# Kernel optimization log

Hardware: AMD Instinct MI355X
Metric: run time of the kernel (lower is better)

## Reference

```python
import math
import jax, jax.numpy as jnp
import numpy as np

B, S, D, H = 2, 2048, 1024, 16
HD = D // H


def setup_inputs() -> dict:
    key = jax.random.key(0)
    ks = jax.random.split(key, 12)
    w = lambda k: jax.random.normal(k, (D, D), jnp.float32) * 0.02
    return {
        "query": jax.random.normal(ks[0], (B, S, D), jnp.float32),
        "key": jax.random.normal(ks[1], (B, S, D), jnp.float32),
        "value": jax.random.normal(ks[2], (B, S, D), jnp.float32),
        "mask": jax.random.randint(ks[3], (B, 1, S, S), 0, 2, jnp.int32),
        "relative_pos_bias": jax.random.normal(ks[4], (S, S, H), jnp.float32) * 0.1,
        "Wq": w(ks[5]), "bq": jnp.zeros((D,), jnp.float32),
        "Wk": w(ks[6]), "bk": jnp.zeros((D,), jnp.float32),
        "Wv": w(ks[7]), "bv": jnp.zeros((D,), jnp.float32),
        "Wo": w(ks[8]), "bo": jnp.zeros((D,), jnp.float32),
    }


def reference(query, key, value, mask, relative_pos_bias,
              Wq, bq, Wk, bk, Wv, bv, Wo, bo):
    b, s, d = query.shape
    h = relative_pos_bias.shape[-1]
    hd = d // h
    scale = math.sqrt(hd)
    # projections -> (b, h, s, hd)
    split = lambda x: x.reshape(b, s, h, hd).transpose(0, 2, 1, 3)
    Q = split(query @ Wq + bq)
    K = split(key @ Wk + bk)
    V = split(value @ Wv + bv)
    scores = jnp.einsum("bhqd,bhkd->bhqk", Q, K) / scale
    # torch: bias.unsqueeze(0).transpose(1,3) => scores[b,h,i,j] += bias[j,i,h]
    scores = scores + jnp.transpose(relative_pos_bias, (2, 1, 0))[None]
    scores = jnp.where(mask == 0, jnp.float32(-1e9), scores)
    attn = jax.nn.softmax(scores, axis=-1)
    out = jnp.einsum("bhqk,bhkd->bhqd", attn, V)
    out = out.transpose(0, 2, 1, 3).reshape(b, s, d)
    return out @ Wo + bo
```

## Files before the change

kernel.cpp:

```cpp
#include <hip/hip_runtime.h>
#include <math.h>

#define SS 2048
#define DD 1024
#define HH 16

typedef _Float16 f16;
typedef _Float16 half8 __attribute__((ext_vector_type(8)));
typedef _Float16 half4 __attribute__((ext_vector_type(4)));
typedef float f32x4 __attribute__((ext_vector_type(4)));
typedef unsigned long long u64;

#define LOG2E 1.44269504f
#define MASKNEG -30000.0f

__device__ __forceinline__ void gload16(const void* g, void* lds) {
    __builtin_amdgcn_global_load_lds(
        (const __attribute__((address_space(1))) unsigned int*)g,
        (__attribute__((address_space(3))) unsigned int*)lds, 16, 0, 0);
}

__global__ __launch_bounds__(256)
void prep_xw(const float* __restrict__ q, const float* __restrict__ k,
             const float* __restrict__ v, f16* __restrict__ oq,
             f16* __restrict__ ok, f16* __restrict__ ov,
             const float* __restrict__ wq, const float* __restrict__ wk,
             const float* __restrict__ wv, const float* __restrict__ wo,
             f16* __restrict__ owq, f16* __restrict__ owk,
             f16* __restrict__ owv, f16* __restrict__ owo)
{
    __shared__ __align__(16) char smem[16640];
    const int bid = blockIdx.x;
    const int t = threadIdx.x;
    if (bid < 6144) {
        const int z = bid / 2048, bx = bid % 2048;
        const float* src = z == 0 ? q : z == 1 ? k : v;
        f16* dst = z == 0 ? oq : z == 1 ? ok : ov;
        size_t i = ((size_t)bx * 256 + t) * 8;
        float4 v0 = *reinterpret_cast<const float4*>(src + i);
        float4 v1 = *reinterpret_cast<const float4*>(src + i + 4);
        half8 h;
        h[0] = (f16)v0.x; h[1] = (f16)v0.y; h[2] = (f16)v0.z; h[3] = (f16)v0.w;
        h[4] = (f16)v1.x; h[5] = (f16)v1.y; h[6] = (f16)v1.z; h[7] = (f16)v1.w;
        *reinterpret_cast<half8*>(dst + i) = h;
    } else {
        const int r = bid - 6144;
        const int z = r / 256;
        const int bx = r % 16, by = (r / 16) % 16;
        const float* W = z == 0 ? wq : z == 1 ? wk : z == 2 ? wv : wo;
        f16* WT = z == 0 ? owq : z == 1 ? owk : z == 2 ? owv : owo;
        float (*Lt)[65] = (float (*)[65])smem;
        const int n0 = bx * 64, k0 = by * 64;
        {
            int row = t >> 2;
            int c0  = (t & 3) * 16;
#pragma unroll
            for (int u = 0; u < 4; ++u) {
                float4 x = *reinterpret_cast<const float4*>(
                    &W[(size_t)(k0 + row) * DD + n0 + c0 + u * 4]);
                Lt[row][c0 + u * 4 + 0] = x.x;
                Lt[row][c0 + u * 4 + 1] = x.y;
                Lt[row][c0 + u * 4 + 2] = x.z;
                Lt[row][c0 + u * 4 + 3] = x.w;
            }
        }
        __syncthreads();
        {
            int n  = t >> 2;
            int kc = (t & 3) * 16;
            half8 h0, h1;
#pragma unroll
            for (int u = 0; u < 8; ++u) h0[u] = (f16)Lt[kc + u][n];
#pragma unroll
            for (int u = 0; u < 8; ++u) h1[u] = (f16)Lt[kc + 8 + u][n];
            f16* dst = &WT[(size_t)(n0 + n) * DD + k0 + kc];
            *reinterpret_cast<half8*>(dst) = h0;
            *reinterpret_cast<half8*>(dst + 8) = h1;
        }
    }
}

__device__ void proj3_body(char* smem, int gx, int gy, int gz,
                           const f16* Xq, const f16* Xk, const f16* Xv,
                           const f16* WqT, const f16* WkT, const f16* WvT,
                           const float* bq, const float* bk, const float* bv,
                           f16* Qo, f16* Ko, f16* VTo)
{
    char* AsB = smem;
    char* BsB = smem + 128 * 64 * 2;
    const int t = threadIdx.x, wid = t >> 6, l = t & 63, c = l & 15, g = l >> 4;
    const f16 *Ap, *Bp; const float* bias; int m0, n0;
    if (gz == 2) { Ap = WvT; Bp = Xv; bias = bv; m0 = gx * 128; n0 = gy * 128; }
    else if (gz == 1) { Ap = Xk; Bp = WkT; bias = bk; m0 = gy * 128; n0 = gx * 128; }
    else { Ap = Xq; Bp = WqT; bias = bq; m0 = gy * 128; n0 = gx * 128; }
    const int wm = wid >> 1, wn = wid & 1;
    f32x4 acc[4][4] = {};

    const int s  = l & 7;
    const int r0 = wid * 32 + (l >> 3);
    const int sdst = (s << 4) ^ ((r0 & 7) << 4);

    half8 aN[4], bN[4];
#pragma unroll
    for (int j = 0; j < 4; ++j) {
        int row = r0 + j * 8;
        aN[j] = *(const half8*)(Ap + (size_t)(m0 + row) * DD + s * 8);
        bN[j] = *(const half8*)(Bp + (size_t)(n0 + row) * DD + s * 8);
    }
#pragma unroll
    for (int j = 0; j < 4; ++j) {
        int row = r0 + j * 8;
        *(half8*)(AsB + row * 128 + sdst) = aN[j];
        *(half8*)(BsB + row * 128 + sdst) = bN[j];
    }
    __syncthreads();

    for (int k0 = 0; k0 < DD; k0 += 64) {
        const bool more = (k0 + 64 < DD);
        const int kn = more ? k0 + 64 : 0;
#pragma unroll
        for (int j = 0; j < 4; ++j) {
            int row = r0 + j * 8;
            aN[j] = *(const half8*)(Ap + (size_t)(m0 + row) * DD + kn + s * 8);
            bN[j] = *(const half8*)(Bp + (size_t)(n0 + row) * DD + kn + s * 8);
        }
#pragma unroll
        for (int ks = 0; ks < 2; ++ks) {
            half8 af[4];
#pragma unroll
            for (int mt = 0; mt < 4; ++mt) {
                int row = wm * 64 + mt * 16 + c;
                af[mt] = *(const half8*)(AsB + row * 128 +
                         ((ks * 64 + g * 16) ^ ((row & 7) << 4)));
            }
#pragma unroll
            for (int nt = 0; nt < 4; ++nt) {
                int row = wn * 64 + nt * 16 + c;
                half8 bf = *(const half8*)(BsB + row * 128 +
                           ((ks * 64 + g * 16) ^ ((row & 7) << 4)));
#pragma unroll
                for (int mt = 0; mt < 4; ++mt)
                    acc[mt][nt] = __builtin_amdgcn_mfma_f32_16x16x32_f16(
                        af[mt], bf, acc[mt][nt], 0, 0, 0);
            }
        }
        __syncthreads();
        if (more) {
#pragma unroll
            for (int j = 0; j < 4; ++j) {
                int row = r0 + j * 8;
                *(half8*)(AsB + row * 128 + sdst) = aN[j];
                *(half8*)(BsB + row * 128 + sdst) = bN[j];
            }
        }
        __syncthreads();
    }

    f16* Ls = (f16*)smem;
    const float post = (gz == 0) ? 0.125f * LOG2E : 1.0f;
    if (gz < 2) {
#pragma unroll
        for (int nt = 0; nt < 4; ++nt) {
            int col = wn * 64 + nt * 16 + c;
            float bn = bias[n0 + col];
#pragma unroll
            for (int mt = 0; mt < 4; ++mt)
#pragma unroll
                for (int reg = 0; reg < 4; ++reg) {
                    int row = wm * 64 + mt * 16 + 4 * g + reg;
                    Ls[row * 128 + (col ^ ((row & 7) << 3))] =
                        (f16)((acc[mt][nt][reg] + bn) * post);
                }
        }
    } else {
#pragma unroll
        for (int mt = 0; mt < 4; ++mt)
#pragma unroll
            for (int reg = 0; reg < 4; ++reg) {
                int row = wm * 64 + mt * 16 + 4 * g + reg;
                float bd = bias[m0 + row];
#pragma unroll
                for (int nt = 0; nt < 4; ++nt) {
                    int col = wn * 64 + nt * 16 + c;
                    Ls[row * 128 + (col ^ ((row & 7) << 3))] =
                        (f16)(acc[mt][nt][reg] + bd);
                }
            }
    }
    __syncthreads();
#pragma unroll
    for (int e = 0; e < 8; ++e) {
        int fi = e * 256 + t;
        int row = fi >> 4;
        int col0 = (fi & 15) * 8;
        half8 v = *reinterpret_cast<const half8*>(
            Ls + row * 128 + (col0 ^ ((row & 7) << 3)));
        if (gz < 2) {
            f16* dst = gz ? Ko : Qo;
            int m = m0 + row, n = n0 + col0;
            int b = m >> 11, sdx = m & (SS - 1);
            int h = n >> 6, hd = n & 63;
            *reinterpret_cast<half8*>(
                &dst[(((size_t)(b * HH + h)) * SS + sdx) * 64 + hd]) = v;
        } else {
            int m = m0 + row, n = n0 + col0;
            int h = m >> 6, dl = m & 63;
            int b = n >> 11;
            *reinterpret_cast<half8*>(
                &VTo[(((size_t)(b * HH + h)) * 64 + dl) * SS + (n & (SS - 1))]) = v;
        }
    }
}

__device__ void rpbT3_body(char* smem, int gxi, int gyj,
                           const float* rpb, f16* rpbT)
{
    f16* Lt = (f16*)smem;
    const int t = threadIdx.x, wid = t >> 6, l = t & 63;
    const int i0 = gxi * 16;
    const int j0 = gyj * 64;
    const int il = l >> 2;
    const int h0 = (l & 3) * 4;
    const int swz = (il & 7) << 3;
#pragma unroll
    for (int p = 0; p < 16; ++p) {
        int jl = p * 4 + wid;
        float4 v = *reinterpret_cast<const float4*>(
            rpb + ((size_t)(j0 + jl) * SS + i0 + il) * HH + h0);
        int js = jl ^ swz;
        Lt[((h0 + 0) * 16 + il) * 64 + js] = (f16)(v.x * LOG2E);
        Lt[((h0 + 1) * 16 + il) * 64 + js] = (f16)(v.y * LOG2E);
        Lt[((h0 + 2) * 16 + il) * 64 + js] = (f16)(v.z * LOG2E);
        Lt[((h0 + 3) * 16 + il) * 64 + js] = (f16)(v.w * LOG2E);
    }
    __syncthreads();
    const int part = t & 7;
#pragma unroll
    for (int p = 0; p < 8; ++p) {
        int rowid = p * 32 + (t >> 3);
        int h = rowid >> 4, i2 = rowid & 15;
        int rsw = (i2 & 7) << 3;
        const f16* rowp = Lt + (h * 16 + i2) * 64;
        half8 v;
#pragma unroll
        for (int e = 0; e < 8; ++e) {
            int sig = 32 * (part & 1) + 16 * (e >> 2) + 4 * (part >> 1) + (e & 3);
            v[e] = rowp[sig ^ rsw];
        }
        *reinterpret_cast<half8*>(
            rpbT + ((size_t)h * SS + i0 + i2) * SS + j0 + part * 8) = v;
    }
}

__device__ void maskbits_body(int gx, const int* mask, u64* mb)
{
    const int t = threadIdx.x, wid = t >> 6, l = t & 63;
    const int row = gx * 4 + wid;
    const int* src = mask + (size_t)row * SS;
    u64* dst = mb + (size_t)row * 32;
    for (int it = 0; it < 32; ++it) {
        int mv = src[it * 64 + l];
        u64 bal = __ballot(mv != 0);
        if (l == 0) dst[it] = bal;
    }
}

__global__ __launch_bounds__(256)
void prep_big(const f16* __restrict__ Xq, const f16* __restrict__ Xk,
              const f16* __restrict__ Xv, const f16* __restrict__ WqT,
              const f16* __restrict__ WkT, const f16* __restrict__ WvT,
              const float* __restrict__ bq, const float* __restrict__ bk,
              const float* __restrict__ bv,
              f16* __restrict__ Qo, f16* __restrict__ Ko, f16* __restrict__ VTo,
              const float* __restrict__ rpb, f16* __restrict__ rpbT,
              const int* __restrict__ mask, u64* __restrict__ mbits)
{
    __shared__ __align__(16) char smem[32768];
    const int bid = blockIdx.x;
    const int pid0 = (int)(((long long)bid * 768) / 5888);
    const int pid1 = (int)(((long long)(bid + 1) * 768) / 5888);
    if (pid1 != pid0) {
        proj3_body(smem, pid0 % 8, (pid0 / 8) % 32, pid0 / 256,
                   Xq, Xk, Xv, WqT, WkT, WvT, bq, bk, bv, Qo, Ko, VTo);
    } else {
        const int mid = bid - pid0;
        if (mid < 4096)
            rpbT3_body(smem, mid % 128, mid / 128, rpb, rpbT);
        else
            maskbits_body(mid - 4096, mask, mbits);
    }
}

__global__ __launch_bounds__(256, 4)
void attn_fwd(const f16* __restrict__ Qw, const f16* __restrict__ Kw,
              const f16* __restrict__ VTw, const f16* __restrict__ rpbT,
              const u64* __restrict__ mbits, f16* __restrict__ AOh)
{
    __shared__ f16 Ks[2][64 * 64];
    __shared__ f16 Vs[2][64 * 64];

    const int t = threadIdx.x, wid = t >> 6, l = t & 63, c = l & 15, g = l >> 4;
    const int bh = blockIdx.x, b = bh >> 4, h = bh & 15;
    const int q0 = blockIdx.y * 64;
    const size_t baseSD = (size_t)bh * SS * 64;
    const size_t baseDS = (size_t)bh * 64 * SS;
    const f16* Kbase = Kw + baseSD;
    const f16* Vbase = VTw + baseDS;

    const int qrow_c = q0 + wid * 16 + c;
    const f16* bp = rpbT + (size_t)h * SS * SS + (size_t)qrow_c * SS + g * 16;
    const u64* mp = mbits + ((size_t)b * SS + qrow_c) * 32;

    const int s     = l & 7;
    const int srow0 = wid * 16 + (l >> 3);
    const int sswz  = (srow0 & 7) << 4;
    const int kdst  = (s << 4) ^ sswz;
    const int velo  = 32 * (s >> 2) + 16 * (s & 1) + 4 * ((s >> 1) & 1);
    const int vdlo  = (velo * 2) ^ sswz;
    const int vdhi  = (velo * 2 + 16) ^ sswz;

    int ga[4];
#pragma unroll
    for (int r = 0; r < 4; ++r) ga[r] = (g * 4 + r) * 4;

    half8 qf[2];
    qf[0] = *(const half8*)(Qw + baseSD + (size_t)qrow_c * 64 + g * 8);
    qf[1] = *(const half8*)(Qw + baseSD + (size_t)qrow_c * 64 + 32 + g * 8);

    {
        half8 k0 = *(const half8*)(Kbase + (size_t)srow0 * 64 + s * 8);
        half8 k1 = *(const half8*)(Kbase + (size_t)(srow0 + 8) * 64 + s * 8);
        half8 v0 = *(const half8*)(Vbase + (size_t)srow0 * SS + s * 8);
        half8 v1 = *(const half8*)(Vbase + (size_t)(srow0 + 8) * SS + s * 8);
        char* kd = (char*)Ks[0]; char* vd = (char*)Vs[0];
        *(half8*)(kd + srow0 * 128 + kdst) = k0;
        *(half8*)(kd + (srow0 + 8) * 128 + kdst) = k1;
        half4 lo0 = {v0[0], v0[1], v0[2], v0[3]}, hi0 = {v0[4], v0[5], v0[6], v0[7]};
        half4 lo1 = {v1[0], v1[1], v1[2], v1[3]}, hi1 = {v1[4], v1[5], v1[6], v1[7]};
        *(half4*)(vd + srow0 * 128 + vdlo) = lo0;
        *(half4*)(vd + srow0 * 128 + vdhi) = hi0;
        *(half4*)(vd + (srow0 + 8) * 128 + vdlo) = lo1;
        *(half4*)(vd + (srow0 + 8) * 128 + vdhi) = hi1;
    }
    half8 bb0 = *(const half8*)(bp);
    half8 bb1 = *(const half8*)(bp + 8);
    u64 mm = mp[0];
    __syncthreads();

    f32x4 acc[4] = {};
    float mrow = -INFINITY, lp = 0.f;
    const int shg = 4 * g;

    int buf = 0;
    for (int kt = 0; kt < SS / 64; ++kt) {
        const bool more = (kt + 1 < SS / 64);
        const int jn = more ? (kt + 1) * 64 : 0;
        const int ktn = more ? kt + 1 : 0;

        half8 k0n = *(const half8*)(Kbase + (size_t)(jn + srow0) * 64 + s * 8);
        half8 k1n = *(const half8*)(Kbase + (size_t)(jn + srow0 + 8) * 64 + s * 8);
        half8 v0n = *(const half8*)(Vbase + (size_t)srow0 * SS + jn + s * 8);
        half8 v1n = *(const half8*)(Vbase + (size_t)(srow0 + 8) * SS + jn + s * 8);
        half8 bbn0 = *(const half8*)(bp + jn);
        half8 bbn1 = *(const half8*)(bp + jn + 8);
        u64 mmn = mp[ktn];

        char* KsB = (char*)Ks[buf];
        char* VsB = (char*)Vs[buf];

        u64 sh = mm >> shg;
        f32x4 sc[4];
#pragma unroll
        for (int nt = 0; nt < 4; ++nt)
#pragma unroll
            for (int r = 0; r < 4; ++r) {
                float bf = (float)(nt < 2 ? bb0[nt * 4 + r] : bb1[(nt - 2) * 4 + r]);
                sc[nt][r] = ((sh >> (16 * nt + r)) & 1) ? bf : MASKNEG;
            }

        __builtin_amdgcn_s_setprio(1);
#pragma unroll
        for (int ks = 0; ks < 2; ++ks)
#pragma unroll
            for (int nt = 0; nt < 4; ++nt) {
                int row = nt * 16 + c;
                half8 kf = *(const half8*)(KsB + row * 128 +
                           ((ks * 64 + g * 16) ^ ((row & 7) << 4)));
                sc[nt] = __builtin_amdgcn_mfma_f32_16x16x32_f16(
                    kf, qf[ks], sc[nt], 0, 0, 0);
            }
        __builtin_amdgcn_s_setprio(0);

        float rm = fmaxf(fmaxf(fmaxf(sc[0][0], sc[0][1]), fmaxf(sc[0][2], sc[0][3])),
                         fmaxf(fmaxf(sc[1][0], sc[1][1]), fmaxf(sc[1][2], sc[1][3])));
        rm = fmaxf(rm, fmaxf(fmaxf(fmaxf(sc[2][0], sc[2][1]), fmaxf(sc[2][2], sc[2][3])),
                             fmaxf(fmaxf(sc[3][0], sc[3][1]), fmaxf(sc[3][2], sc[3][3]))));
        rm = fmaxf(rm, __shfl_xor(rm, 16));
        rm = fmaxf(rm, __shfl_xor(rm, 32));
        if (!__all(rm <= mrow + 8.0f)) {
            float mn = fmaxf(mrow, rm);
            float scal = exp2f(mrow - mn);
            mrow = mn;
            lp *= scal;
            float sq[4];
#pragma unroll
            for (int r = 0; r < 4; ++r)
                sq[r] = __int_as_float(__builtin_amdgcn_ds_bpermute(
                            ga[r], __float_as_int(scal)));
#pragma unroll
            for (int nt = 0; nt < 4; ++nt)
#pragma unroll
                for (int r = 0; r < 4; ++r) acc[nt][r] *= sq[r];
        }
        float psum = 0.f;
#pragma unroll
        for (int nt = 0; nt < 4; ++nt)
#pragma unroll
            for (int r = 0; r < 4; ++r) {
                float p = exp2f(sc[nt][r] - mrow);
                sc[nt][r] = p;
                psum += p;
            }
        lp += psum;

        half4 pa[4];
#pragma unroll
        for (int kk = 0; kk < 4; ++kk) {
            half4 pv = {(f16)sc[kk][0], (f16)sc[kk][1],
                        (f16)sc[kk][2], (f16)sc[kk][3]};
            pa[kk] = pv;
        }

        __builtin_amdgcn_s_setprio(1);
#pragma unroll
        for (int ks = 0; ks < 2; ++ks)
#pragma unroll
            for (int nt2 = 0; nt2 < 4; ++nt2) {
                int row = nt2 * 16 + c;
                half8 vf = *(const half8*)(VsB + row * 128 +
                           ((ks * 64 + g * 16) ^ ((row & 7) << 4)));
                half4 vlo = {vf[0], vf[1], vf[2], vf[3]};
                half4 vhi = {vf[4], vf[5], vf[6], vf[7]};
                acc[nt2] = __builtin_amdgcn_mfma_f32_16x16x16f16(
                    pa[2 * ks], vlo, acc[nt2], 0, 0, 0);
                acc[nt2] = __builtin_amdgcn_mfma_f32_16x16x16f16(
                    pa[2 * ks + 1], vhi, acc[nt2], 0, 0, 0);
            }
        __builtin_amdgcn_s_setprio(0);

        if (more) {
            char* kd = (char*)Ks[buf ^ 1];
            char* vd = (char*)Vs[buf ^ 1];
            *(half8*)(kd + srow0 * 128 + kdst) = k0n;
            *(half8*)(kd + (srow0 + 8) * 128 + kdst) = k1n;
            half4 lo0 = {v0n[0], v0n[1], v0n[2], v0n[3]}, hi0 = {v0n[4], v0n[5], v0n[6], v0n[7]};
            half4 lo1 = {v1n[0], v1n[1], v1n[2], v1n[3]}, hi1 = {v1n[4], v1n[5], v1n[6], v1n[7]};
            *(half4*)(vd + srow0 * 128 + vdlo) = lo0;
            *(half4*)(vd + srow0 * 128 + vdhi) = hi0;
            *(half4*)(vd + (srow0 + 8) * 128 + vdlo) = lo1;
            *(half4*)(vd + (srow0 + 8) * 128 + vdhi) = hi1;
            buf ^= 1;
            bb0 = bbn0; bb1 = bbn1; mm = mmn;
        }
        __syncthreads();
    }

    float lt = lp;
    lt += __shfl_xor(lt, 16);
    lt += __shfl_xor(lt, 32);
    float linv[4];
#pragma unroll
    for (int r = 0; r < 4; ++r)
        linv[r] = 1.0f / __int_as_float(__builtin_amdgcn_ds_bpermute(
                      ga[r], __float_as_int(lt)));
#pragma unroll
    for (int r = 0; r < 4; ++r) {
        int qrow = q0 + wid * 16 + 4 * g + r;
#pragma unroll
        for (int nt2 = 0; nt2 < 4; ++nt2)
            AOh[((size_t)b * SS + qrow) * DD + h * 64 + nt2 * 16 + c] =
                (f16)(acc[nt2][r] * linv[r]);
    }
}

__global__ __launch_bounds__(256)
void gemm_out(const f16* __restrict__ A, const f16* __restrict__ BT,
              const float* __restrict__ bias, float* __restrict__ out)
{
    __shared__ f16 As[128 * 64];
    __shared__ f16 Bs[128 * 64];
    const int t = threadIdx.x, wid = t >> 6, l = t & 63, c = l & 15, g = l >> 4;
    const int m0 = blockIdx.y * 128, n0 = blockIdx.x * 128;
    const int wm = wid >> 1, wn = wid & 1;
    f32x4 acc[4][4] = {};
    char* AsB = (char*)As; char* BsB = (char*)Bs;

    for (int k0 = 0; k0 < DD; k0 += 64) {
        __syncthreads();
#pragma unroll
        for (int j = 0; j < 4; ++j) {
            int row = wid * 32 + j * 8 + (l >> 3);
            int slot = (l & 7) ^ (row & 7);
            gload16(A + (size_t)(m0 + row) * DD + k0 + slot * 8,
                    AsB + (wid * 32 + j * 8) * 128);
            gload16(BT + (size_t)(n0 + row) * DD + k0 + slot * 8,
                    BsB + (wid * 32 + j * 8) * 128);
        }
        __syncthreads();
#pragma unroll
        for (int ks = 0; ks < 2; ++ks) {
            half8 af[4];
#pragma unroll
            for (int mt = 0; mt < 4; ++mt) {
                int row = wm * 64 + mt * 16 + c;
                af[mt] = *(const half8*)(AsB + row * 128 +
                         ((ks * 64 + g * 16) ^ ((row & 7) << 4)));
            }
#pragma unroll
            for (int nt = 0; nt < 4; ++nt) {
                int row = wn * 64 + nt * 16 + c;
                half8 bf = *(const half8*)(BsB + row * 128 +
                           ((ks * 64 + g * 16) ^ ((row & 7) << 4)));
#pragma unroll
                for (int mt = 0; mt < 4; ++mt)
                    acc[mt][nt] = __builtin_amdgcn_mfma_f32_16x16x32_f16(
                        af[mt], bf, acc[mt][nt], 0, 0, 0);
            }
        }
    }
#pragma unroll
    for (int nt = 0; nt < 4; ++nt) {
        int n = n0 + wn * 64 + nt * 16 + c;
        float bn = bias[n];
#pragma unroll
        for (int mt = 0; mt < 4; ++mt)
#pragma unroll
            for (int reg = 0; reg < 4; ++reg) {
                int m = m0 + wm * 64 + mt * 16 + 4 * g + reg;
                out[(size_t)m * DD + n] = acc[mt][nt][reg] + bn;
            }
    }
}

extern "C" void kernel_launch(void* const* d_in, const int* in_sizes, int n_in,
                              void* d_out, int out_size, void* d_ws, size_t ws_size,
                              hipStream_t stream)
{
    (void)in_sizes; (void)n_in; (void)out_size; (void)ws_size;

    const float* query = (const float*)d_in[0];
    const float* key   = (const float*)d_in[1];
    const float* value = (const float*)d_in[2];
    const int*   mask  = (const int*)d_in[3];
    const float* rpb   = (const float*)d_in[4];
    const float* Wq = (const float*)d_in[5];  const float* bq = (const float*)d_in[6];
    const float* Wk = (const float*)d_in[7];  const float* bk = (const float*)d_in[8];
    const float* Wv = (const float*)d_in[9];  const float* bv = (const float*)d_in[10];
    const float* Wo = (const float*)d_in[11]; const float* bo = (const float*)d_in[12];
    float* out = (float*)d_out;

    const size_t NX = (size_t)2 * SS * DD;
    const size_t NW = (size_t)DD * DD;
    f16* Xq    = (f16*)d_ws;
    f16* Xk    = Xq + NX;
    f16* Xv    = Xk + NX;
    f16* WqT   = Xv + NX;
    f16* WkT   = WqT + NW;
    f16* WvT   = WkT + NW;
    f16* WoT   = WvT + NW;
    f16* Qw    = WoT + NW;
    f16* Kw    = Qw + NX;
    f16* VTw   = Kw + NX;
    f16* rpbT  = VTw + NX;
    u64* mbits = (u64*)(rpbT + (size_t)HH * SS * SS);
    f16* AOh   = Xq;

    prep_xw<<<dim3(7168), 256, 0, stream>>>(query, key, value, Xq, Xk, Xv,
                                            Wq, Wk, Wv, Wo, WqT, WkT, WvT, WoT);
    prep_big<<<dim3(5888), 256, 0, stream>>>(Xq, Xk, Xv, WqT, WkT, WvT,
                                             bq, bk, bv, Qw, Kw, VTw,
                                             rpb, rpbT, mask, mbits);
    attn_fwd<<<dim3(2 * HH, SS / 64), 256, 0, stream>>>(Qw, Kw, VTw, rpbT, mbits, AOh);
    gemm_out<<<dim3(8, 32), 256, 0, stream>>>(AOh, WoT, bo, out);
}
```

Before: 284.9 us.

## Regroup prep kernels: move rpb/mask prep to memory pass, standalone projection GEMM

The rpb transpose and mask bit-packing work moves out of the mixed projection kernel and into the first memory-bound prep kernel. The QKV projection GEMM becomes its own launch with a 3D grid, so MFMA blocks no longer interleave with bandwidth-bound blocks. The GEMM inner loop also raises wave priority around the MFMA section. The trade-off is that the GEMM no longer overlaps with the rpb and mask traffic, and the first kernel now carries all the memory-bound work.

```diff
diff --git a/kernel.cpp b/kernel.cpp
--- a/kernel.cpp
+++ b/kernel.cpp
@@ -20,20 +20,78 @@
         (__attribute__((address_space(3))) unsigned int*)lds, 16, 0, 0);
 }
 
+__device__ void rpbT3_body(char* smem, int gxi, int gyj,
+                           const float* rpb, f16* rpbT)
+{
+    f16* Lt = (f16*)smem;
+    const int t = threadIdx.x, wid = t >> 6, l = t & 63;
+    const int i0 = gxi * 16;
+    const int j0 = gyj * 64;
+    const int il = l >> 2;
+    const int h0 = (l & 3) * 4;
+    const int swz = (il & 7) << 3;
+#pragma unroll
+    for (int p = 0; p < 16; ++p) {
+        int jl = p * 4 + wid;
+        float4 v = *reinterpret_cast<const float4*>(
+            rpb + ((size_t)(j0 + jl) * SS + i0 + il) * HH + h0);
+        int js = jl ^ swz;
+        Lt[((h0 + 0) * 16 + il) * 64 + js] = (f16)(v.x * LOG2E);
+        Lt[((h0 + 1) * 16 + il) * 64 + js] = (f16)(v.y * LOG2E);
+        Lt[((h0 + 2) * 16 + il) * 64 + js] = (f16)(v.z * LOG2E);
+        Lt[((h0 + 3) * 16 + il) * 64 + js] = (f16)(v.w * LOG2E);
+    }
+    __syncthreads();
+    const int part = t & 7;
+#pragma unroll
+    for (int p = 0; p < 8; ++p) {
+        int rowid = p * 32 + (t >> 3);
+        int h = rowid >> 4, i2 = rowid & 15;
+        int rsw = (i2 & 7) << 3;
+        const f16* rowp = Lt + (h * 16 + i2) * 64;
+        half8 v;
+#pragma unroll
+        for (int e = 0; e < 8; ++e) {
+            int sig = 32 * (part & 1) + 16 * (e >> 2) + 4 * (part >> 1) + (e & 3);
+            v[e] = rowp[sig ^ rsw];
+        }
+        *reinterpret_cast<half8*>(
+            rpbT + ((size_t)h * SS + i0 + i2) * SS + j0 + part * 8) = v;
+    }
+}
+
+__device__ void maskbits_body(int gx, const int* mask, u64* mb)
+{
+    const int t = threadIdx.x, wid = t >> 6, l = t & 63;
+    const int row = gx * 4 + wid;
+    const int* src = mask + (size_t)row * SS;
+    u64* dst = mb + (size_t)row * 32;
+    for (int it = 0; it < 32; ++it) {
+        int mv = src[it * 64 + l];
+        u64 bal = __ballot(mv != 0);
+        if (l == 0) dst[it] = bal;
+    }
+}
+
 __global__ __launch_bounds__(256)
-void prep_xw(const float* __restrict__ q, const float* __restrict__ k,
-             const float* __restrict__ v, f16* __restrict__ oq,
-             f16* __restrict__ ok, f16* __restrict__ ov,
-             const float* __restrict__ wq, const float* __restrict__ wk,
-             const float* __restrict__ wv, const float* __restrict__ wo,
-             f16* __restrict__ owq, f16* __restrict__ owk,
-             f16* __restrict__ owv, f16* __restrict__ owo)
-{
-    __shared__ __align__(16) char smem[16640];
+void prep_mem(const float* __restrict__ q, const float* __restrict__ k,
+              const float* __restrict__ v, f16* __restrict__ oq,
+              f16* __restrict__ ok, f16* __restrict__ ov,
+              const float* __restrict__ wq, const float* __restrict__ wk,
+              const float* __restrict__ wv, const float* __restrict__ wo,
+              f16* __restrict__ owq, f16* __restrict__ owk,
+              f16* __restrict__ owv, f16* __restrict__ owo,
+              const float* __restrict__ rpb, f16* __restrict__ rpbT,
+              const int* __restrict__ mask, u64* __restrict__ mbits)
+{
+    __shared__ __align__(16) char smem[32768];
     const int bid = blockIdx.x;
     const int t = threadIdx.x;
-    if (bid < 6144) {
-        const int z = bid / 2048, bx = bid % 2048;
+    if (bid < 4096) {
+        rpbT3_body(smem, bid % 128, bid / 128, rpb, rpbT);
+    } else if (bid < 4096 + 6144) {
+        const int r = bid - 4096;
+        const int z = r / 2048, bx = r % 2048;
         const float* src = z == 0 ? q : z == 1 ? k : v;
         f16* dst = z == 0 ? oq : z == 1 ? ok : ov;
         size_t i = ((size_t)bx * 256 + t) * 8;
@@ -43,8 +101,8 @@
         h[0] = (f16)v0.x; h[1] = (f16)v0.y; h[2] = (f16)v0.z; h[3] = (f16)v0.w;
         h[4] = (f16)v1.x; h[5] = (f16)v1.y; h[6] = (f16)v1.z; h[7] = (f16)v1.w;
         *reinterpret_cast<half8*>(dst + i) = h;
-    } else {
-        const int r = bid - 6144;
+    } else if (bid < 4096 + 6144 + 1024) {
+        const int r = bid - (4096 + 6144);
         const int z = r / 256;
         const int bx = r % 16, by = (r / 16) % 16;
         const float* W = z == 0 ? wq : z == 1 ? wk : z == 2 ? wv : wo;
@@ -77,17 +135,23 @@
             *reinterpret_cast<half8*>(dst) = h0;
             *reinterpret_cast<half8*>(dst + 8) = h1;
         }
-    }
-}
-
-__device__ void proj3_body(char* smem, int gx, int gy, int gz,
-                           const f16* Xq, const f16* Xk, const f16* Xv,
-                           const f16* WqT, const f16* WkT, const f16* WvT,
-                           const float* bq, const float* bk, const float* bv,
-                           f16* Qo, f16* Ko, f16* VTo)
-{
+    } else {
+        maskbits_body(bid - (4096 + 6144 + 1024), mask, mbits);
+    }
+}
+
+__global__ __launch_bounds__(256)
+void proj3(const f16* __restrict__ Xq, const f16* __restrict__ Xk,
+           const f16* __restrict__ Xv, const f16* __restrict__ WqT,
+           const f16* __restrict__ WkT, const f16* __restrict__ WvT,
+           const float* __restrict__ bq, const float* __restrict__ bk,
+           const float* __restrict__ bv,
+           f16* __restrict__ Qo, f16* __restrict__ Ko, f16* __restrict__ VTo)
+{
+    __shared__ __align__(16) char smem[32768];
     char* AsB = smem;
     char* BsB = smem + 128 * 64 * 2;
+    const int gx = blockIdx.x, gy = blockIdx.y, gz = blockIdx.z;
     const int t = threadIdx.x, wid = t >> 6, l = t & 63, c = l & 15, g = l >> 4;
     const f16 *Ap, *Bp; const float* bias; int m0, n0;
     if (gz == 2) { Ap = WvT; Bp = Xv; bias = bv; m0 = gx * 128; n0 = gy * 128; }
@@ -124,6 +188,7 @@
             aN[j] = *(const half8*)(Ap + (size_t)(m0 + row) * DD + kn + s * 8);
             bN[j] = *(const half8*)(Bp + (size_t)(n0 + row) * DD + kn + s * 8);
         }
+        __builtin_amdgcn_s_setprio(1);
 #pragma unroll
         for (int ks = 0; ks < 2; ++ks) {
             half8 af[4];
@@ -144,6 +209,7 @@
                         af[mt], bf, acc[mt][nt], 0, 0, 0);
             }
         }
+        __builtin_amdgcn_s_setprio(0);
         __syncthreads();
         if (more) {
 #pragma unroll
@@ -212,85 +278,6 @@
     }
 }
 
-__device__ void rpbT3_body(char* smem, int gxi, int gyj,
-                           const float* rpb, f16* rpbT)
-{
-    f16* Lt = (f16*)smem;
-    const int t = threadIdx.x, wid = t >> 6, l = t & 63;
-    const int i0 = gxi * 16;
-    const int j0 = gyj * 64;
-    const int il = l >> 2;
-    const int h0 = (l & 3) * 4;
-    const int swz = (il & 7) << 3;
-#pragma unroll
-    for (int p = 0; p < 16; ++p) {
-        int jl = p * 4 + wid;
-        float4 v = *reinterpret_cast<const float4*>(
-            rpb + ((size_t)(j0 + jl) * SS + i0 + il) * HH + h0);
-        int js = jl ^ swz;
-        Lt[((h0 + 0) * 16 + il) * 64 + js] = (f16)(v.x * LOG2E);
-        Lt[((h0 + 1) * 16 + il) * 64 + js] = (f16)(v.y * LOG2E);
-        Lt[((h0 + 2) * 16 + il) * 64 + js] = (f16)(v.z * LOG2E);
-        Lt[((h0 + 3) * 16 + il) * 64 + js] = (f16)(v.w * LOG2E);
-    }
-    __syncthreads();
-    const int part = t & 7;
-#pragma unroll
-    for (int p = 0; p < 8; ++p) {
-        int rowid = p * 32 + (t >> 3);
-        int h = rowid >> 4, i2 = rowid & 15;
-        int rsw = (i2 & 7) << 3;
-        const f16* rowp = Lt + (h * 16 + i2) * 64;
-        half8 v;
-#pragma unroll
-        for (int e = 0; e < 8; ++e) {
-            int sig = 32 * (part & 1) + 16 * (e >> 2) + 4 * (part >> 1) + (e & 3);
-            v[e] = rowp[sig ^ rsw];
-        }
-        *reinterpret_cast<half8*>(
-            rpbT + ((size_t)h * SS + i0 + i2) * SS + j0 + part * 8) = v;
-    }
-}
-
-__device__ void maskbits_body(int gx, const int* mask, u64* mb)
-{
-    const int t = threadIdx.x, wid = t >> 6, l = t & 63;
-    const int row = gx * 4 + wid;
-    const int* src = mask + (size_t)row * SS;
-    u64* dst = mb + (size_t)row * 32;
-    for (int it = 0; it < 32; ++it) {
-        int mv = src[it * 64 + l];
-        u64 bal = __ballot(mv != 0);
-        if (l == 0) dst[it] = bal;
-    }
-}
-
-__global__ __launch_bounds__(256)
-void prep_big(const f16* __restrict__ Xq, const f16* __restrict__ Xk,
-              const f16* __restrict__ Xv, const f16* __restrict__ WqT,
-              const f16* __restrict__ WkT, const f16* __restrict__ WvT,
-              const float* __restrict__ bq, const float* __restrict__ bk,
-              const float* __restrict__ bv,
-              f16* __restrict__ Qo, f16* __restrict__ Ko, f16* __restrict__ VTo,
-              const float* __restrict__ rpb, f16* __restrict__ rpbT,
-              const int* __restrict__ mask, u64* __restrict__ mbits)
-{
-    __shared__ __align__(16) char smem[32768];
-    const int bid = blockIdx.x;
-    const int pid0 = (int)(((long long)bid * 768) / 5888);
-    const int pid1 = (int)(((long long)(bid + 1) * 768) / 5888);
-    if (pid1 != pid0) {
-        proj3_body(smem, pid0 % 8, (pid0 / 8) % 32, pid0 / 256,
-                   Xq, Xk, Xv, WqT, WkT, WvT, bq, bk, bv, Qo, Ko, VTo);
-    } else {
-        const int mid = bid - pid0;
-        if (mid < 4096)
-            rpbT3_body(smem, mid % 128, mid / 128, rpb, rpbT);
-        else
-            maskbits_body(mid - 4096, mask, mbits);
-    }
-}
-
 __global__ __launch_bounds__(256, 4)
 void attn_fwd(const f16* __restrict__ Qw, const f16* __restrict__ Kw,
               const f16* __restrict__ VTw, const f16* __restrict__ rpbT,
@@ -575,11 +562,11 @@
     u64* mbits = (u64*)(rpbT + (size_t)HH * SS * SS);
     f16* AOh   = Xq;
 
-    prep_xw<<<dim3(7168), 256, 0, stream>>>(query, key, value, Xq, Xk, Xv,
-                                            Wq, Wk, Wv, Wo, WqT, WkT, WvT, WoT);
-    prep_big<<<dim3(5888), 256, 0, stream>>>(Xq, Xk, Xv, WqT, WkT, WvT,
-                                             bq, bk, bv, Qw, Kw, VTw,
-                                             rpb, rpbT, mask, mbits);
+    prep_mem<<<dim3(12288), 256, 0, stream>>>(query, key, value, Xq, Xk, Xv,
+                                              Wq, Wk, Wv, Wo, WqT, WkT, WvT, WoT,
+                                              rpb, rpbT, mask, mbits);
+    proj3<<<dim3(8, 32, 3), 256, 0, stream>>>(Xq, Xk, Xv, WqT, WkT, WvT,
+                                              bq, bk, bv, Qw, Kw, VTw);
     attn_fwd<<<dim3(2 * HH, SS / 64), 256, 0, stream>>>(Qw, Kw, VTw, rpbT, mbits, AOh);
     gemm_out<<<dim3(8, 32), 256, 0, stream>>>(AOh, WoT, bo, out);
 }
```

Result: faster. 276.9 us, median of 2 (-2.8%).
